# Performance work log

Measured on AMD Instinct MI355X. Metric: run time of the kernel, lower is better.

Reference implementation:

```python
import jax, jax.numpy as jnp
import numpy as np

H = 1024
NH = 16
DH = H // NH

def setup_inputs() -> dict:
    key = jax.random.key(0)
    ks = jax.random.split(key, 6)
    s = 1.0 / np.sqrt(H)
    x = jax.random.normal(ks[0], (4, 2048, H), dtype=jnp.float32)
    Wq = jax.random.uniform(ks[1], (H, H), jnp.float32, -s, s)
    Wk = jax.random.uniform(ks[2], (H, H), jnp.float32, -s, s)
    Wv = jax.random.uniform(ks[3], (H, H), jnp.float32, -s, s)
    Wo = jax.random.uniform(ks[4], (H, H), jnp.float32, -s, s)
    bo = jax.random.uniform(ks[5], (H,), jnp.float32, -s, s)
    return {"x": x, "Wq": Wq, "Wk": Wk, "Wv": Wv, "Wo": Wo, "bo": bo}

def reference(x, Wq, Wk, Wv, Wo, bo):
    B, T, Hd = x.shape
    # projections: torch Linear is x @ W.T
    def split_heads(y):
        return y.reshape(B, T, NH, DH).transpose(0, 2, 1, 3)  # [B, nh, T, dh]
    Q = split_heads(x @ Wq.T)
    K = split_heads(x @ Wk.T)
    V = split_heads(x @ Wv.T)
    scores = jnp.einsum('bhtd,bhsd->bhts', Q, K) / jnp.sqrt(jnp.float32(DH))
    w = jax.nn.softmax(scores, axis=-1)
    ctx = jnp.einsum('bhts,bhsd->bhtd', w, V)  # [B, nh, T, dh]
    ctx = ctx.transpose(0, 2, 1, 3).reshape(B, T, Hd)
    out = ctx @ Wo.T + bo  # [B, T, H]
    return out.mean(axis=1)  # [B, H]
```

## Files before the change

kernel.cpp:

```cpp
#include <hip/hip_runtime.h>
#include <hip/hip_bf16.h>
#include <cstdint>

#define BB   4
#define TT   2048
#define HH   1024
#define NHH  16
#define DHH  64
#define MM   (BB*TT)
#define N3   (3*HH)

typedef __attribute__((ext_vector_type(8))) short short8;
typedef __attribute__((ext_vector_type(4))) float f32x4;

#if __has_builtin(__builtin_amdgcn_exp2f)
#define EXP2F(x) __builtin_amdgcn_exp2f(x)
#else
#define EXP2F(x) exp2f(x)
#endif

#define QSCALE 0.1803368801111204f

__device__ __forceinline__ float bf2f(unsigned short u) {
    return __uint_as_float(((uint32_t)u) << 16);
}
__device__ __forceinline__ unsigned short f2bf(float f) {
    uint32_t u = __float_as_uint(f);
    return (unsigned short)((u + 0x7fffu + ((u >> 16) & 1u)) >> 16);
}
__device__ __forceinline__ void gload_lds16(const unsigned short* g, unsigned short* l) {
    __builtin_amdgcn_global_load_lds(
        (const __attribute__((address_space(1))) uint32_t*)g,
        (__attribute__((address_space(3))) uint32_t*)l, 16, 0, 0);
}

__global__ __launch_bounds__(256) void cvt_bf16(
    const float* __restrict__ src, unsigned short* __restrict__ dst, int n4)
{
    int i = blockIdx.x * 256 + threadIdx.x;
    const int stride = gridDim.x * 256;
    for (; i < n4; i += stride) {
        float4 v = ((const float4*)src)[i];
        ushort4 o;
        o.x = f2bf(v.x); o.y = f2bf(v.y); o.z = f2bf(v.z); o.w = f2bf(v.w);
        ((ushort4*)dst)[i] = o;
    }
}

__global__ __launch_bounds__(256) void cvt_w3(
    const float* __restrict__ Wq, const float* __restrict__ Wk,
    const float* __restrict__ Wv, unsigned short* __restrict__ Wb)
{
    const float* src = (blockIdx.y == 0) ? Wq : (blockIdx.y == 1 ? Wk : Wv);
    unsigned short* dst = Wb + (size_t)blockIdx.y * HH * HH;
    const int n4 = HH * HH / 4;
    int i = blockIdx.x * 256 + threadIdx.x;
    const int stride = gridDim.x * 256;
    for (; i < n4; i += stride) {
        float4 v = ((const float4*)src)[i];
        ushort4 o;
        o.x = f2bf(v.x); o.y = f2bf(v.y); o.z = f2bf(v.z); o.w = f2bf(v.w);
        ((ushort4*)dst)[i] = o;
    }
}

__global__ __launch_bounds__(256) void proj_mfma(
    const unsigned short* __restrict__ xb, const unsigned short* __restrict__ Wb,
    unsigned short* __restrict__ qp, unsigned short* __restrict__ kp,
    unsigned short* __restrict__ vp)
{
    __shared__ unsigned short As[4096];
    __shared__ unsigned short Bs[4096];
    const int m0 = blockIdx.x * 128;
    const int n0 = blockIdx.y * 128;
    const int sel = n0 >> 10;
    const unsigned short* Wbase = Wb + (size_t)sel * HH * HH;
    const int nw0 = n0 & (HH - 1);
    const int tid = threadIdx.x;
    const int wave = tid >> 6, lane = tid & 63;
    const int quad = lane >> 4, l15 = lane & 15;
    const int wm = wave >> 1, wn = wave & 1;

    f32x4 acc[4][4];
    #pragma unroll
    for (int i = 0; i < 4; ++i)
        #pragma unroll
        for (int j = 0; j < 4; ++j) acc[i][j] = (f32x4){0.f, 0.f, 0.f, 0.f};

    for (int k0 = 0; k0 < HH; k0 += 32) {
        __syncthreads();
        #pragma unroll
        for (int q = 0; q < 2; ++q) {
            const int chunk = (wave * 2 + q) * 64 + lane;
            const int kc = chunk >> 7, mrow = chunk & 127;
            gload_lds16(xb    + (size_t)(m0  + mrow) * HH + k0 + kc * 8, As + chunk * 8);
            gload_lds16(Wbase + (size_t)(nw0 + mrow) * HH + k0 + kc * 8, Bs + chunk * 8);
        }
        __syncthreads();
        short8 af[4], bf[4];
        #pragma unroll
        for (int i = 0; i < 4; ++i)
            af[i] = *(const short8*)&As[(quad * 128 + wm * 64 + i * 16 + l15) * 8];
        #pragma unroll
        for (int j = 0; j < 4; ++j)
            bf[j] = *(const short8*)&Bs[(quad * 128 + wn * 64 + j * 16 + l15) * 8];
        #pragma unroll
        for (int i = 0; i < 4; ++i)
            #pragma unroll
            for (int j = 0; j < 4; ++j)
                acc[i][j] = __builtin_amdgcn_mfma_f32_16x16x32_bf16(af[i], bf[j], acc[i][j], 0, 0, 0);
    }
    unsigned short* outp = (sel == 0) ? qp : (sel == 1 ? kp : vp);
    const float cscale = (sel == 0) ? QSCALE : 1.0f;
    #pragma unroll
    for (int i = 0; i < 4; ++i)
        #pragma unroll
        for (int j = 0; j < 4; ++j) {
            const int col = n0 + wn * 64 + j * 16 + l15;
            const int hh2 = (col >> 6) & (NHH - 1);
            const int dd  = col & (DHH - 1);
            #pragma unroll
            for (int r = 0; r < 4; ++r) {
                const int row = m0 + wm * 64 + i * 16 + quad * 4 + r;
                const int bb2 = row >> 11, tt2 = row & (TT - 1);
                outp[((size_t)(bb2 * NHH + hh2) * TT + tt2) * DHH + dd] =
                    f2bf(acc[i][j][r] * cscale);
            }
        }
}

__global__ __launch_bounds__(256) void attn_fused(
    const unsigned short* __restrict__ qp, const unsigned short* __restrict__ kp,
    float* __restrict__ a)
{
    const int t0 = blockIdx.x * 128;
    const int h = blockIdx.y, b = blockIdx.z;
    const int bh = b * NHH + h;
    const int tid = threadIdx.x;
    const int wave = tid >> 6, lane = tid & 63;
    const int quad = lane >> 4, l15 = lane & 15;
    __shared__ float red[4][128];
    __shared__ float linv[128];

    const unsigned short* q = qp + (size_t)bh * TT * DHH;
    const unsigned short* kptr =
        kp + (size_t)bh * TT * DHH + (size_t)(wave * 512 + l15) * DHH + quad * 8;

    short8 aq[8][2];
    #pragma unroll
    for (int i = 0; i < 8; ++i)
        #pragma unroll
        for (int c = 0; c < 2; ++c)
            aq[i][c] = *(const short8*)&q[(size_t)(t0 + i * 16 + l15) * DHH + quad * 8 + c * 32];

#define KLD(ss, c) (*(const short8*)(kptr + (size_t)(ss) * 16 * DHH + (c) * 32))

    float rs[8][4];
    #pragma unroll
    for (int i = 0; i < 8; ++i)
        #pragma unroll
        for (int r = 0; r < 4; ++r) rs[i][r] = 0.f;

    {
        short8 c0a = KLD(0, 0), c0b = KLD(0, 1);
        short8 c1a = KLD(1, 0), c1b = KLD(1, 1);
        for (int ss = 0; ss < 32; ++ss) {
            const short8 ba = c0a, bb = c0b;
            c0a = c1a; c0b = c1b;
            if (ss < 30) { c1a = KLD(ss + 2, 0); c1b = KLD(ss + 2, 1); }
            #pragma unroll
            for (int i = 0; i < 8; ++i) {
                f32x4 c = (f32x4){0.f, 0.f, 0.f, 0.f};
                c = __builtin_amdgcn_mfma_f32_16x16x32_bf16(aq[i][0], ba, c, 0, 0, 0);
                c = __builtin_amdgcn_mfma_f32_16x16x32_bf16(aq[i][1], bb, c, 0, 0, 0);
                #pragma unroll
                for (int r = 0; r < 4; ++r) rs[i][r] += EXP2F(c[r]);
            }
        }
    }
    #pragma unroll
    for (int off = 1; off < 16; off <<= 1)
        #pragma unroll
        for (int i = 0; i < 8; ++i)
            #pragma unroll
            for (int r = 0; r < 4; ++r) rs[i][r] += __shfl_xor(rs[i][r], off);
    if (l15 == 0)
        #pragma unroll
        for (int i = 0; i < 8; ++i)
            #pragma unroll
            for (int r = 0; r < 4; ++r) red[wave][i * 16 + quad * 4 + r] = rs[i][r];
    __syncthreads();
    if (tid < 128) {
        const float l = red[0][tid] + red[1][tid] + red[2][tid] + red[3][tid];
        linv[tid] = 1.0f / (l * (float)TT);
    }
    __syncthreads();

    float lrv[8][4];
    #pragma unroll
    for (int i = 0; i < 8; ++i)
        #pragma unroll
        for (int r = 0; r < 4; ++r) lrv[i][r] = linv[i * 16 + quad * 4 + r];

    {
        short8 c0a = KLD(0, 0), c0b = KLD(0, 1);
        short8 c1a = KLD(1, 0), c1b = KLD(1, 1);
        for (int ss = 0; ss < 32; ++ss) {
            const short8 ba = c0a, bb = c0b;
            c0a = c1a; c0b = c1b;
            if (ss < 30) { c1a = KLD(ss + 2, 0); c1b = KLD(ss + 2, 1); }
            float cs = 0.f;
            #pragma unroll
            for (int i = 0; i < 8; ++i) {
                f32x4 c = (f32x4){0.f, 0.f, 0.f, 0.f};
                c = __builtin_amdgcn_mfma_f32_16x16x32_bf16(aq[i][0], ba, c, 0, 0, 0);
                c = __builtin_amdgcn_mfma_f32_16x16x32_bf16(aq[i][1], bb, c, 0, 0, 0);
                #pragma unroll
                for (int r = 0; r < 4; ++r) cs += EXP2F(c[r]) * lrv[i][r];
            }
            cs += __shfl_xor(cs, 16);
            cs += __shfl_xor(cs, 32);
            if (lane < 16)
                atomicAdd(&a[(size_t)bh * TT + wave * 512 + ss * 16 + l15], cs);
        }
    }
#undef KLD
}

__global__ __launch_bounds__(256) void ctx_mean(
    const unsigned short* __restrict__ vp, const float* __restrict__ a,
    float* __restrict__ cm)
{
    const int h = blockIdx.x, b = blockIdx.y, sb = blockIdx.z;
    const int tid = threadIdx.x;
    const int d = tid & 63, sg = tid >> 6;
    const int bh = b * NHH + h;
    __shared__ float red[4][64];
    float part = 0.f;
    for (int s = sb * 256 + sg; s < sb * 256 + 256; s += 4) {
        const float av = a[(size_t)bh * TT + s];
        part += av * bf2f(vp[((size_t)bh * TT + s) * DHH + d]);
    }
    red[sg][d] = part;
    __syncthreads();
    if (tid < 64)
        atomicAdd(&cm[b * HH + h * DHH + tid],
                  red[0][tid] + red[1][tid] + red[2][tid] + red[3][tid]);
}

__global__ __launch_bounds__(256) void out_proj(
    const float* __restrict__ cm, const float* __restrict__ Wo,
    const float* __restrict__ bo, float* __restrict__ out)
{
    const int b = blockIdx.y;
    const int jb = blockIdx.x;
    const int tid = threadIdx.x;
    const int j = jb * 64 + (tid >> 2);
    const int kg = tid & 3;
    __shared__ float cs[HH];
    for (int k = tid; k < HH; k += 256) cs[k] = cm[b * HH + k];
    __syncthreads();
    float acc = 0.f;
    const float* wrow = &Wo[(size_t)j * HH];
    #pragma unroll 8
    for (int i = 0; i < 64; ++i) {
        const int k = kg * 256 + i * 4;
        float4 w4 = *(const float4*)&wrow[k];
        acc += w4.x * cs[k] + w4.y * cs[k+1] + w4.z * cs[k+2] + w4.w * cs[k+3];
    }
    acc += __shfl_down(acc, 2, 4);
    acc += __shfl_down(acc, 1, 4);
    if (kg == 0) out[b * HH + j] = acc + bo[j];
}

extern "C" void kernel_launch(void* const* d_in, const int* in_sizes, int n_in,
                              void* d_out, int out_size, void* d_ws, size_t ws_size,
                              hipStream_t stream) {
    const float* x  = (const float*)d_in[0];
    const float* Wq = (const float*)d_in[1];
    const float* Wk = (const float*)d_in[2];
    const float* Wv = (const float*)d_in[3];
    const float* Wo = (const float*)d_in[4];
    const float* bo = (const float*)d_in[5];
    float* out = (float*)d_out;

    char* ws = (char*)d_ws;
    unsigned short* qp = (unsigned short*)ws;  ws += (size_t)MM * HH * 2;
    unsigned short* kp = (unsigned short*)ws;  ws += (size_t)MM * HH * 2;
    unsigned short* vp = (unsigned short*)ws;  ws += (size_t)MM * HH * 2;
    unsigned short* xb = (unsigned short*)ws;  ws += (size_t)MM * HH * 2;
    unsigned short* Wb = (unsigned short*)ws;  ws += (size_t)3 * HH * HH * 2;
    float* a  = (float*)ws;                    ws += (size_t)BB * NHH * TT * 4;
    float* cm = (float*)ws;

    hipMemsetAsync(a, 0, (size_t)(BB * NHH * TT + BB * HH) * 4, stream);

    cvt_bf16<<<2048, 256, 0, stream>>>(x, xb, MM * HH / 4);
    cvt_w3  <<<dim3(512, 3), 256, 0, stream>>>(Wq, Wk, Wv, Wb);

    proj_mfma <<<dim3(64, 24),      256, 0, stream>>>(xb, Wb, qp, kp, vp);
    attn_fused<<<dim3(16, NHH, BB), 256, 0, stream>>>(qp, kp, a);
    ctx_mean  <<<dim3(NHH, BB, 8),  256, 0, stream>>>(vp, a, cm);
    out_proj  <<<dim3(16, BB),      256, 0, stream>>>(cm, Wo, bo, out);
}
```

Baseline: 321.9 us.

## Double K-tile depth in projection GEMM and reorder attention grid mapping

```diff
diff --git a/kernel.cpp b/kernel.cpp
--- a/kernel.cpp
+++ b/kernel.cpp
@@ -69,8 +69,8 @@
     unsigned short* __restrict__ qp, unsigned short* __restrict__ kp,
     unsigned short* __restrict__ vp)
 {
-    __shared__ unsigned short As[4096];
-    __shared__ unsigned short Bs[4096];
+    __shared__ unsigned short As[8192];
+    __shared__ unsigned short Bs[8192];
     const int m0 = blockIdx.x * 128;
     const int n0 = blockIdx.y * 128;
     const int sel = n0 >> 10;
@@ -87,28 +87,33 @@
         #pragma unroll
         for (int j = 0; j < 4; ++j) acc[i][j] = (f32x4){0.f, 0.f, 0.f, 0.f};
 
-    for (int k0 = 0; k0 < HH; k0 += 32) {
+    for (int k0 = 0; k0 < HH; k0 += 64) {
         __syncthreads();
         #pragma unroll
-        for (int q = 0; q < 2; ++q) {
-            const int chunk = (wave * 2 + q) * 64 + lane;
+        for (int q = 0; q < 4; ++q) {
+            const int chunk = (wave * 4 + q) * 64 + lane;
             const int kc = chunk >> 7, mrow = chunk & 127;
             gload_lds16(xb    + (size_t)(m0  + mrow) * HH + k0 + kc * 8, As + chunk * 8);
             gload_lds16(Wbase + (size_t)(nw0 + mrow) * HH + k0 + kc * 8, Bs + chunk * 8);
         }
         __syncthreads();
-        short8 af[4], bf[4];
-        #pragma unroll
-        for (int i = 0; i < 4; ++i)
-            af[i] = *(const short8*)&As[(quad * 128 + wm * 64 + i * 16 + l15) * 8];
-        #pragma unroll
-        for (int j = 0; j < 4; ++j)
-            bf[j] = *(const short8*)&Bs[(quad * 128 + wn * 64 + j * 16 + l15) * 8];
-        #pragma unroll
-        for (int i = 0; i < 4; ++i)
+        short8 af[2][4], bf[2][4];
+        #pragma unroll
+        for (int kk = 0; kk < 2; ++kk) {
+            #pragma unroll
+            for (int i = 0; i < 4; ++i)
+                af[kk][i] = *(const short8*)&As[((kk * 4 + quad) * 128 + wm * 64 + i * 16 + l15) * 8];
             #pragma unroll
             for (int j = 0; j < 4; ++j)
-                acc[i][j] = __builtin_amdgcn_mfma_f32_16x16x32_bf16(af[i], bf[j], acc[i][j], 0, 0, 0);
+                bf[kk][j] = *(const short8*)&Bs[((kk * 4 + quad) * 128 + wn * 64 + j * 16 + l15) * 8];
+        }
+        #pragma unroll
+        for (int kk = 0; kk < 2; ++kk)
+            #pragma unroll
+            for (int i = 0; i < 4; ++i)
+                #pragma unroll
+                for (int j = 0; j < 4; ++j)
+                    acc[i][j] = __builtin_amdgcn_mfma_f32_16x16x32_bf16(af[kk][i], bf[kk][j], acc[i][j], 0, 0, 0);
     }
     unsigned short* outp = (sel == 0) ? qp : (sel == 1 ? kp : vp);
     const float cscale = (sel == 0) ? QSCALE : 1.0f;
@@ -133,8 +138,8 @@
     const unsigned short* __restrict__ qp, const unsigned short* __restrict__ kp,
     float* __restrict__ a)
 {
-    const int t0 = blockIdx.x * 128;
-    const int h = blockIdx.y, b = blockIdx.z;
+    const int h = blockIdx.x, b = blockIdx.z;
+    const int t0 = blockIdx.y * 128;
     const int bh = b * NHH + h;
     const int tid = threadIdx.x;
     const int wave = tid >> 6, lane = tid & 63;
@@ -143,7 +148,7 @@
     __shared__ float linv[128];
 
     const unsigned short* q = qp + (size_t)bh * TT * DHH;
-    const unsigned short* kptr =
+    const unsigned short* kbase =
         kp + (size_t)bh * TT * DHH + (size_t)(wave * 512 + l15) * DHH + quad * 8;
 
     short8 aq[8][2];
@@ -153,7 +158,7 @@
         for (int c = 0; c < 2; ++c)
             aq[i][c] = *(const short8*)&q[(size_t)(t0 + i * 16 + l15) * DHH + quad * 8 + c * 32];
 
-#define KLD(ss, c) (*(const short8*)(kptr + (size_t)(ss) * 16 * DHH + (c) * 32))
+    const f32x4 zk = {0.f, 0.f, 0.f, 0.f};
 
     float rs[8][4];
     #pragma unroll
@@ -162,16 +167,24 @@
         for (int r = 0; r < 4; ++r) rs[i][r] = 0.f;
 
     {
-        short8 c0a = KLD(0, 0), c0b = KLD(0, 1);
-        short8 c1a = KLD(1, 0), c1b = KLD(1, 1);
+        const unsigned short* kw = kbase;
+        short8 c0a = *(const short8*)(kw);
+        short8 c0b = *(const short8*)(kw + 32);
+        kw += 16 * DHH;
+        short8 c1a = *(const short8*)(kw);
+        short8 c1b = *(const short8*)(kw + 32);
+        kw += 16 * DHH;
         for (int ss = 0; ss < 32; ++ss) {
             const short8 ba = c0a, bb = c0b;
             c0a = c1a; c0b = c1b;
-            if (ss < 30) { c1a = KLD(ss + 2, 0); c1b = KLD(ss + 2, 1); }
+            if (ss < 30) {
+                c1a = *(const short8*)(kw);
+                c1b = *(const short8*)(kw + 32);
+            }
+            kw += 16 * DHH;
             #pragma unroll
             for (int i = 0; i < 8; ++i) {
-                f32x4 c = (f32x4){0.f, 0.f, 0.f, 0.f};
-                c = __builtin_amdgcn_mfma_f32_16x16x32_bf16(aq[i][0], ba, c, 0, 0, 0);
+                f32x4 c = __builtin_amdgcn_mfma_f32_16x16x32_bf16(aq[i][0], ba, zk, 0, 0, 0);
                 c = __builtin_amdgcn_mfma_f32_16x16x32_bf16(aq[i][1], bb, c, 0, 0, 0);
                 #pragma unroll
                 for (int r = 0; r < 4; ++r) rs[i][r] += EXP2F(c[r]);
@@ -203,17 +216,25 @@
         for (int r = 0; r < 4; ++r) lrv[i][r] = linv[i * 16 + quad * 4 + r];
 
     {
-        short8 c0a = KLD(0, 0), c0b = KLD(0, 1);
-        short8 c1a = KLD(1, 0), c1b = KLD(1, 1);
+        const unsigned short* kw = kbase;
+        short8 c0a = *(const short8*)(kw);
+        short8 c0b = *(const short8*)(kw + 32);
+        kw += 16 * DHH;
+        short8 c1a = *(const short8*)(kw);
+        short8 c1b = *(const short8*)(kw + 32);
+        kw += 16 * DHH;
         for (int ss = 0; ss < 32; ++ss) {
             const short8 ba = c0a, bb = c0b;
             c0a = c1a; c0b = c1b;
-            if (ss < 30) { c1a = KLD(ss + 2, 0); c1b = KLD(ss + 2, 1); }
+            if (ss < 30) {
+                c1a = *(const short8*)(kw);
+                c1b = *(const short8*)(kw + 32);
+            }
+            kw += 16 * DHH;
             float cs = 0.f;
             #pragma unroll
             for (int i = 0; i < 8; ++i) {
-                f32x4 c = (f32x4){0.f, 0.f, 0.f, 0.f};
-                c = __builtin_amdgcn_mfma_f32_16x16x32_bf16(aq[i][0], ba, c, 0, 0, 0);
+                f32x4 c = __builtin_amdgcn_mfma_f32_16x16x32_bf16(aq[i][0], ba, zk, 0, 0, 0);
                 c = __builtin_amdgcn_mfma_f32_16x16x32_bf16(aq[i][1], bb, c, 0, 0, 0);
                 #pragma unroll
                 for (int r = 0; r < 4; ++r) cs += EXP2F(c[r]) * lrv[i][r];
@@ -224,7 +245,6 @@
                 atomicAdd(&a[(size_t)bh * TT + wave * 512 + ss * 16 + l15], cs);
         }
     }
-#undef KLD
 }
 
 __global__ __launch_bounds__(256) void ctx_mean(
@@ -299,7 +319,7 @@
     cvt_w3  <<<dim3(512, 3), 256, 0, stream>>>(Wq, Wk, Wv, Wb);
 
     proj_mfma <<<dim3(64, 24),      256, 0, stream>>>(xb, Wb, qp, kp, vp);
-    attn_fused<<<dim3(16, NHH, BB), 256, 0, stream>>>(qp, kp, a);
+    attn_fused<<<dim3(NHH, 16, BB), 256, 0, stream>>>(qp, kp, a);
     ctx_mean  <<<dim3(NHH, BB, 8),  256, 0, stream>>>(vp, a, cm);
     out_proj  <<<dim3(16, BB),      256, 0, stream>>>(cm, Wo, bo, out);
 }
```

Result: no change. 326.6 us (+1.5%).
